# Optimization experiments

Measured on AMD Instinct MI355X. Metric: run time of the kernel, lower is better.

## Reference

```python
import jax, jax.numpy as jnp
import numpy as np

B, T, C = 16, 4096, 64  # batch, seq_len, n_embd == head_size


def setup_inputs() -> dict:
    key = jax.random.key(0)
    k1, k2, k3, k4 = jax.random.split(key, 4)
    x = jax.random.normal(k1, (B, T, C), dtype=jnp.float32)
    Wq = jax.random.normal(k2, (C, C), dtype=jnp.float32) * (C ** -0.5)
    Wk = jax.random.normal(k3, (C, C), dtype=jnp.float32) * (C ** -0.5)
    Wv = jax.random.normal(k4, (C, C), dtype=jnp.float32) * (C ** -0.5)
    return {"x": x, "Wq": Wq, "Wk": Wk, "Wv": Wv}


def reference(x, Wq, Wk, Wv):
    # Single-head causal self-attention (dropout rate = 0.0 in source -> identity).
    q = jnp.einsum('btc,cd->btd', x, Wq)  # [B,T,D]
    k = jnp.einsum('btc,cd->btd', x, Wk)  # [B,T,D]
    v = jnp.einsum('btc,cd->btd', x, Wv)  # [B,T,D]
    scale = q.shape[-1] ** -0.5
    wei = jnp.einsum('btd,bsd->bts', q, k) * scale  # [B,T,T] scores
    causal = jnp.tril(jnp.ones((T, T), dtype=bool))  # [T,T]
    wei = jnp.where(causal[None, :, :], wei, jnp.finfo(wei.dtype).min)
    wei = jax.nn.softmax(wei, axis=-1)
    out = jnp.einsum('bts,bsd->btd', wei, v)  # [B,T,D]
    return out
```

## Files before the change

### kernel.cpp

```cpp
#include <hip/hip_runtime.h>
#include <hip/hip_bf16.h>
#include <math.h>

#define BATCH 16
#define SEQ 4096
#define HDIM 64

typedef __attribute__((ext_vector_type(8))) short bf16x8;
typedef __attribute__((ext_vector_type(4))) float f32x4;
typedef __attribute__((ext_vector_type(4))) unsigned int u32x4;
typedef __attribute__((ext_vector_type(8))) unsigned short us8;

#define QSCALE 0.1803368801111601f

static __device__ __forceinline__ float exp2_fast(float x) {
#if __has_builtin(__builtin_amdgcn_exp2f)
    return __builtin_amdgcn_exp2f(x);
#else
    float r; asm("v_exp_f32 %0, %1" : "=v"(r) : "v"(x)); return r;
#endif
}

static __device__ __forceinline__ void load_lds16(const void* g, void* l) {
    __builtin_amdgcn_global_load_lds(
        (const __attribute__((address_space(1))) unsigned int*)g,
        (__attribute__((address_space(3))) unsigned int*)l,
        16, 0, 0);
}

static __device__ __forceinline__ unsigned short bf16bits(float f) {
    __hip_bfloat16 h = __float2bfloat16(f);
    return *(unsigned short*)&h;
}

static __device__ __forceinline__ unsigned int pack_bf16_trunc(float f0, float f1) {
    unsigned int u0 = __builtin_bit_cast(unsigned int, f0);
    unsigned int u1 = __builtin_bit_cast(unsigned int, f1);
#if __has_builtin(__builtin_amdgcn_perm)
    return __builtin_amdgcn_perm(u1, u0, 0x07060302u);
#else
    return (u1 & 0xFFFF0000u) | (u0 >> 16);
#endif
}

__global__ __launch_bounds__(256)
void qkv_mfma_kernel(const float* __restrict__ x,
                     const float* __restrict__ Wq,
                     const float* __restrict__ Wk,
                     const float* __restrict__ Wv,
                     __hip_bfloat16* __restrict__ qb,
                     __hip_bfloat16* __restrict__ kb,
                     __hip_bfloat16* __restrict__ vt) {
    __shared__ __attribute__((aligned(16))) __hip_bfloat16 swt[3 * 64 * 64];
    __shared__ __attribute__((aligned(16))) __hip_bfloat16 sout[64][80];
    const int tid = threadIdx.x;
    const int wv = tid >> 6;
    const int lane = tid & 63;
    const int quad = lane >> 4;
    const int ml = lane & 15;
    const size_t row0 = (size_t)blockIdx.x * 64;
    const int batch = (int)(row0 >> 12);
    const int t0 = (int)(row0 & 4095);

    #pragma unroll
    for (int mat = 0; mat < 3; ++mat) {
        const float* W = (mat == 0) ? Wq : (mat == 1) ? Wk : Wv;
        const float sc = (mat == 0) ? QSCALE : 1.0f;
        #pragma unroll
        for (int c2 = 0; c2 < 2; ++c2) {
            const int chunk = c2 * 256 + tid;
            const int n = chunk & 63;
            const int c = chunk >> 6;
            us8 u;
            #pragma unroll
            for (int j = 0; j < 8; ++j)
                u[j] = bf16bits(W[(c * 8 + j) * HDIM + n] * sc);
            *(us8*)(swt + mat * 4096 + n * 64 + (size_t)(c ^ (n & 7)) * 8) = u;
        }
    }

    bf16x8 a0, a1;
    {
        const float4* xr = (const float4*)(x + (row0 + wv * 16 + ml) * HDIM);
        float4 lo = xr[quad * 2], hi = xr[quad * 2 + 1];
        float t8[8] = {lo.x, lo.y, lo.z, lo.w, hi.x, hi.y, hi.z, hi.w};
        #pragma unroll
        for (int j = 0; j < 8; ++j) a0[j] = (short)bf16bits(t8[j]);
        lo = xr[8 + quad * 2]; hi = xr[9 + quad * 2];
        float u8[8] = {lo.x, lo.y, lo.z, lo.w, hi.x, hi.y, hi.z, hi.w};
        #pragma unroll
        for (int j = 0; j < 8; ++j) a1[j] = (short)bf16bits(u8[j]);
    }
    __syncthreads();

    #pragma unroll
    for (int mat = 0; mat < 3; ++mat) {
        const __hip_bfloat16* wb = swt + mat * 4096;
        f32x4 acc[4];
        #pragma unroll
        for (int nt = 0; nt < 4; ++nt) {
            const int n = nt * 16 + ml;
            const int nx = n & 7;
            const bf16x8 bl = *(const bf16x8*)(wb + (size_t)n * 64 + (size_t)((quad) ^ nx) * 8);
            const bf16x8 bh = *(const bf16x8*)(wb + (size_t)n * 64 + (size_t)((quad + 4) ^ nx) * 8);
            acc[nt] = __builtin_amdgcn_mfma_f32_16x16x32_bf16(a0, bl, (f32x4){0.f,0.f,0.f,0.f}, 0, 0, 0);
            acc[nt] = __builtin_amdgcn_mfma_f32_16x16x32_bf16(a1, bh, acc[nt], 0, 0, 0);
        }

        if (mat < 2) {
            #pragma unroll
            for (int nt = 0; nt < 4; ++nt)
                #pragma unroll
                for (int r = 0; r < 4; ++r)
                    sout[wv * 16 + quad * 4 + r][nt * 16 + ml] = __float2bfloat16(acc[nt][r]);
        } else {
            #pragma unroll
            for (int nt = 0; nt < 4; ++nt)
                #pragma unroll
                for (int r = 0; r < 4; ++r)
                    sout[nt * 16 + ml][(wv >> 1) * 32 + quad * 8 + (wv & 1) * 4 + r] =
                        __float2bfloat16(acc[nt][r]);
        }
        __syncthreads();
        __hip_bfloat16* dst = (mat == 0) ? qb : (mat == 1) ? kb : vt;
        #pragma unroll
        for (int c2 = 0; c2 < 2; ++c2) {
            const int cc = c2 * 256 + tid;
            const int row = cc >> 3, g = cc & 7;
            us8 u = *(const us8*)&sout[row][g * 8];
            if (mat < 2)
                *(us8*)(dst + (row0 + row) * HDIM + g * 8) = u;
            else
                *(us8*)(dst + ((size_t)batch * HDIM + row) * SEQ + t0 + g * 8) = u;
        }
        __syncthreads();
    }
}

__global__ __launch_bounds__(256, 4)
void flash_mfma_kernel(const __hip_bfloat16* __restrict__ qb,
                       const __hip_bfloat16* __restrict__ kbuf,
                       const __hip_bfloat16* __restrict__ vt,
                       float* __restrict__ out) {
    __shared__ __attribute__((aligned(16))) __hip_bfloat16 smem[16384];

    const int tid = threadIdx.x;
    const int wv = tid >> 6;
    const int lane = tid & 63;
    const int quad = lane >> 4;
    const int ml = lane & 15;
    const int mh = wv & 1;
    const int kh = wv >> 1;

    const int id = blockIdx.x;
    const int b = id & 15;
    const int t = id >> 4;
    const int hi2 = t >> 4, mid = t & 15;
    const int qt = (hi2 == 0) ? (63 - mid)
                 : (hi2 == 1) ? (32 + mid)
                 : (hi2 == 2) ? (31 - mid) : mid;
    const int qbw = qt * 64 + mh * 32;
    const size_t bb = (size_t)b * SEQ * HDIM;

    const __hip_bfloat16* Q = qb + bb;
    const __hip_bfloat16* K = kbuf + bb;
    const __hip_bfloat16* VT = vt + bb;

    bf16x8 bq[2][2];
    #pragma unroll
    for (int qi = 0; qi < 2; ++qi)
        #pragma unroll
        for (int h = 0; h < 2; ++h)
            bq[qi][h] = *(const bf16x8*)(Q + (size_t)(qbw + qi * 16 + ml) * HDIM + h * 32 + quad * 8);

    bf16x8 ones8;
    #pragma unroll
    for (int j = 0; j < 8; ++j) ones8[j] = (short)0x3F80;

    f32x4 acc[4][2];
    #pragma unroll
    for (int nt = 0; nt < 4; ++nt)
        #pragma unroll
        for (int qi = 0; qi < 2; ++qi) acc[nt][qi] = (f32x4){0.f, 0.f, 0.f, 0.f};
    f32x4 lacc[2] = {(f32x4){0.f,0.f,0.f,0.f}, (f32x4){0.f,0.f,0.f,0.f}};

    const int s0 = wv * 128 + lane;
    const int s1 = s0 + 64;
    const int r0row = s0 >> 3, r0ch = (s0 & 7) ^ (r0row & 7);
    const int r1row = s1 >> 3, r1ch = (s1 & 7) ^ (r1row & 7);
    const int d0 = (wv * 128) * 8;
    const int d1 = (wv * 128 + 64) * 8;

    int koff[2][2], voff[4];
    #pragma unroll
    for (int kt = 0; kt < 2; ++kt) {
        const int row = kh * 32 + kt * 16 + ml;
        const int rb = row << 3, rxx = row & 7;
        koff[kt][0] = (rb | (quad ^ rxx)) * 8;
        koff[kt][1] = (rb | ((quad + 4) ^ rxx)) * 8;
    }
    #pragma unroll
    for (int nt = 0; nt < 4; ++nt) {
        const int row = nt * 16 + ml;
        const int rb = row << 3, rxx = row & 7;
        voff[nt] = (rb | ((kh * 4 + quad) ^ rxx)) * 8;
    }

    load_lds16(K + (size_t)r0row * HDIM + r0ch * 8, smem + d0);
    load_lds16(K + (size_t)r1row * HDIM + r1ch * 8, smem + d1);
    load_lds16(VT + (size_t)r0row * SEQ + r0ch * 8, smem + 8192 + d0);
    load_lds16(VT + (size_t)r1row * SEQ + r1ch * 8, smem + 8192 + d1);
    asm volatile("s_waitcnt vmcnt(0)" ::: "memory");
    __syncthreads();

    for (int tile = 0; tile < qt; ++tile) {
        const int sel = (tile & 1) * 4096;
        const int nsel = 4096 - sel;
        const __hip_bfloat16* sk = smem + sel;
        const __hip_bfloat16* sv = smem + 8192 + sel;

        const int nk = tile * 64 + 64;
        load_lds16(K + (size_t)(nk + r0row) * HDIM + r0ch * 8, smem + nsel + d0);
        load_lds16(K + (size_t)(nk + r1row) * HDIM + r1ch * 8, smem + nsel + d1);
        load_lds16(VT + (size_t)r0row * SEQ + nk + r0ch * 8, smem + 8192 + nsel + d0);
        load_lds16(VT + (size_t)r1row * SEQ + nk + r1ch * 8, smem + 8192 + nsel + d1);

        bf16x8 kf[2][2], va[4];
        #pragma unroll
        for (int kt = 0; kt < 2; ++kt) {
            kf[kt][0] = *(const bf16x8*)(sk + koff[kt][0]);
            kf[kt][1] = *(const bf16x8*)(sk + koff[kt][1]);
        }
        #pragma unroll
        for (int nt = 0; nt < 4; ++nt)
            va[nt] = *(const bf16x8*)(sv + voff[nt]);

        f32x4 st[2][2];
        __builtin_amdgcn_s_setprio(1);
        #pragma unroll
        for (int kt = 0; kt < 2; ++kt)
            #pragma unroll
            for (int qi = 0; qi < 2; ++qi) {
                st[kt][qi] = __builtin_amdgcn_mfma_f32_16x16x32_bf16(kf[kt][0], bq[qi][0], (f32x4){0.f,0.f,0.f,0.f}, 0, 0, 0);
                st[kt][qi] = __builtin_amdgcn_mfma_f32_16x16x32_bf16(kf[kt][1], bq[qi][1], st[kt][qi], 0, 0, 0);
            }
        __builtin_amdgcn_s_setprio(0);

        bf16x8 p80;
        {
            float pv[8];
            #pragma unroll
            for (int half = 0; half < 2; ++half)
                #pragma unroll
                for (int r = 0; r < 4; ++r)
                    pv[half * 4 + r] = exp2_fast(st[half][0][r]);
            u32x4 pk;
            #pragma unroll
            for (int d = 0; d < 4; ++d)
                pk[d] = pack_bf16_trunc(pv[2 * d], pv[2 * d + 1]);
            p80 = __builtin_bit_cast(bf16x8, pk);
        }

        __builtin_amdgcn_s_setprio(1);
        lacc[0] = __builtin_amdgcn_mfma_f32_16x16x32_bf16(ones8, p80, lacc[0], 0, 0, 0);
        #pragma unroll
        for (int nt = 0; nt < 4; ++nt)
            acc[nt][0] = __builtin_amdgcn_mfma_f32_16x16x32_bf16(va[nt], p80, acc[nt][0], 0, 0, 0);
        __builtin_amdgcn_s_setprio(0);

        bf16x8 p81;
        {
            float pv[8];
            #pragma unroll
            for (int half = 0; half < 2; ++half)
                #pragma unroll
                for (int r = 0; r < 4; ++r)
                    pv[half * 4 + r] = exp2_fast(st[half][1][r]);
            u32x4 pk;
            #pragma unroll
            for (int d = 0; d < 4; ++d)
                pk[d] = pack_bf16_trunc(pv[2 * d], pv[2 * d + 1]);
            p81 = __builtin_bit_cast(bf16x8, pk);
        }

        __builtin_amdgcn_s_setprio(1);
        lacc[1] = __builtin_amdgcn_mfma_f32_16x16x32_bf16(ones8, p81, lacc[1], 0, 0, 0);
        #pragma unroll
        for (int nt = 0; nt < 4; ++nt)
            acc[nt][1] = __builtin_amdgcn_mfma_f32_16x16x32_bf16(va[nt], p81, acc[nt][1], 0, 0, 0);
        __builtin_amdgcn_s_setprio(0);

        asm volatile("s_waitcnt vmcnt(0)" ::: "memory");
        __syncthreads();
    }

    {
        const int kb0 = qt * 64;
        const int sel = (qt & 1) * 4096;
        const __hip_bfloat16* sk = smem + sel;
        const __hip_bfloat16* sv = smem + 8192 + sel;

        if (!(kh == 1 && mh == 0)) {
            bf16x8 kf[2][2], va[4];
            #pragma unroll
            for (int kt = 0; kt < 2; ++kt) {
                kf[kt][0] = *(const bf16x8*)(sk + koff[kt][0]);
                kf[kt][1] = *(const bf16x8*)(sk + koff[kt][1]);
            }
            #pragma unroll
            for (int nt = 0; nt < 4; ++nt)
                va[nt] = *(const bf16x8*)(sv + voff[nt]);

            f32x4 st[2][2];
            #pragma unroll
            for (int kt = 0; kt < 2; ++kt)
                #pragma unroll
                for (int qi = 0; qi < 2; ++qi) {
                    st[kt][qi] = __builtin_amdgcn_mfma_f32_16x16x32_bf16(kf[kt][0], bq[qi][0], (f32x4){0.f,0.f,0.f,0.f}, 0, 0, 0);
                    st[kt][qi] = __builtin_amdgcn_mfma_f32_16x16x32_bf16(kf[kt][1], bq[qi][1], st[kt][qi], 0, 0, 0);
                }

            bf16x8 p8[2];
            #pragma unroll
            for (int qi = 0; qi < 2; ++qi) {
                const int q = qbw + qi * 16 + ml;
                float pv[8];
                #pragma unroll
                for (int half = 0; half < 2; ++half)
                    #pragma unroll
                    for (int r = 0; r < 4; ++r) {
                        const int key = kb0 + kh * 32 + half * 16 + quad * 4 + r;
                        float pval = exp2_fast(st[half][qi][r]);
                        if (key > q) pval = 0.f;
                        pv[half * 4 + r] = pval;
                    }
                u32x4 pk;
                #pragma unroll
                for (int d = 0; d < 4; ++d)
                    pk[d] = pack_bf16_trunc(pv[2 * d], pv[2 * d + 1]);
                p8[qi] = __builtin_bit_cast(bf16x8, pk);
            }

            lacc[0] = __builtin_amdgcn_mfma_f32_16x16x32_bf16(ones8, p8[0], lacc[0], 0, 0, 0);
            lacc[1] = __builtin_amdgcn_mfma_f32_16x16x32_bf16(ones8, p8[1], lacc[1], 0, 0, 0);
            #pragma unroll
            for (int nt = 0; nt < 4; ++nt) {
                acc[nt][0] = __builtin_amdgcn_mfma_f32_16x16x32_bf16(va[nt], p8[0], acc[nt][0], 0, 0, 0);
                acc[nt][1] = __builtin_amdgcn_mfma_f32_16x16x32_bf16(va[nt], p8[1], acc[nt][1], 0, 0, 0);
            }
        }
    }

    float (*smerge)[64][18] = (float (*)[64][18])smem;
    #pragma unroll
    for (int qi = 0; qi < 2; ++qi) {
        __syncthreads();
        if (kh == 1) {
            float* mrow = smerge[mh][lane];
            #pragma unroll
            for (int nt = 0; nt < 4; ++nt)
                #pragma unroll
                for (int r = 0; r < 4; ++r) mrow[nt * 4 + r] = acc[nt][qi][r];
            mrow[16] = lacc[qi][0];
        }
        __syncthreads();
        if (kh == 0) {
            const float* mrow = smerge[mh][lane];
            const float inv = 1.0f / (lacc[qi][0] + mrow[16]);
            float* orow = out + bb + (size_t)(qbw + qi * 16 + ml) * HDIM;
            #pragma unroll
            for (int nt = 0; nt < 4; ++nt) {
                float4 o;
                o.x = (acc[nt][qi][0] + mrow[nt * 4 + 0]) * inv;
                o.y = (acc[nt][qi][1] + mrow[nt * 4 + 1]) * inv;
                o.z = (acc[nt][qi][2] + mrow[nt * 4 + 2]) * inv;
                o.w = (acc[nt][qi][3] + mrow[nt * 4 + 3]) * inv;
                *(float4*)(orow + nt * 16 + quad * 4) = o;
            }
        }
    }
}

extern "C" void kernel_launch(void* const* d_in, const int* in_sizes, int n_in,
                              void* d_out, int out_size, void* d_ws, size_t ws_size,
                              hipStream_t stream) {
    const float* x  = (const float*)d_in[0];
    const float* Wq = (const float*)d_in[1];
    const float* Wk = (const float*)d_in[2];
    const float* Wv = (const float*)d_in[3];
    float* outp = (float*)d_out;

    const size_t elems = (size_t)BATCH * SEQ * HDIM;
    __hip_bfloat16* qb = (__hip_bfloat16*)d_ws;
    __hip_bfloat16* kb = qb + elems;
    __hip_bfloat16* vt = kb + elems;

    qkv_mfma_kernel<<<dim3(BATCH * SEQ / 64), 256, 0, stream>>>(x, Wq, Wk, Wv, qb, kb, vt);
    flash_mfma_kernel<<<dim3(BATCH * SEQ / 64), 256, 0, stream>>>(qb, kb, vt, outp);
}
```

Baseline: 118.3 us.

## Precompute swizzled bf16 weights once and stage x via direct-to-LDS loads

Adds a tiny kernel that converts and swizzles Wq/Wk/Wv into bf16 in the workspace once per call, so the 1024 QKV blocks no longer each redo the strided fp32 weight reads and conversion. Each QKV block now pulls the pre-swizzled weights and its x tile into LDS with global_load_lds, then converts x to bf16 with truncating packs instead of round-to-nearest. This trades an extra kernel launch and one more workspace buffer for cheaper per-block setup, and truncation slightly changes the numerics of the x rounding.

After: 118.7 us. No clear change (+0.3%).

```diff
diff --git a/kernel.cpp b/kernel.cpp
--- a/kernel.cpp
+++ b/kernel.cpp
@@ -44,15 +44,38 @@
 }
 
 __global__ __launch_bounds__(256)
+void wconv_kernel(const float* __restrict__ Wq,
+                  const float* __restrict__ Wk,
+                  const float* __restrict__ Wv,
+                  __hip_bfloat16* __restrict__ wsw) {
+    const int mat = blockIdx.x;
+    const int tid = threadIdx.x;
+    const float* W = (mat == 0) ? Wq : (mat == 1) ? Wk : Wv;
+    const float sc = (mat == 0) ? QSCALE : 1.0f;
+    #pragma unroll
+    for (int c2 = 0; c2 < 2; ++c2) {
+        const int chunk = c2 * 256 + tid;
+        const int n = chunk & 63;
+        const int c = chunk >> 6;
+        us8 u;
+        #pragma unroll
+        for (int j = 0; j < 8; ++j)
+            u[j] = bf16bits(W[(c * 8 + j) * HDIM + n] * sc);
+        *(us8*)(wsw + mat * 4096 + n * 64 + (size_t)(c ^ (n & 7)) * 8) = u;
+    }
+}
+
+__global__ __launch_bounds__(256)
 void qkv_mfma_kernel(const float* __restrict__ x,
-                     const float* __restrict__ Wq,
-                     const float* __restrict__ Wk,
-                     const float* __restrict__ Wv,
+                     const __hip_bfloat16* __restrict__ wsw,
                      __hip_bfloat16* __restrict__ qb,
                      __hip_bfloat16* __restrict__ kb,
                      __hip_bfloat16* __restrict__ vt) {
     __shared__ __attribute__((aligned(16))) __hip_bfloat16 swt[3 * 64 * 64];
-    __shared__ __attribute__((aligned(16))) __hip_bfloat16 sout[64][80];
+    __shared__ __attribute__((aligned(16))) char spool[16384];
+    float* sx = (float*)spool;
+    __hip_bfloat16 (*sout)[80] = (__hip_bfloat16 (*)[80])spool;
+
     const int tid = threadIdx.x;
     const int wv = tid >> 6;
     const int lane = tid & 63;
@@ -63,33 +86,32 @@
     const int t0 = (int)(row0 & 4095);
 
     #pragma unroll
-    for (int mat = 0; mat < 3; ++mat) {
-        const float* W = (mat == 0) ? Wq : (mat == 1) ? Wk : Wv;
-        const float sc = (mat == 0) ? QSCALE : 1.0f;
-        #pragma unroll
-        for (int c2 = 0; c2 < 2; ++c2) {
-            const int chunk = c2 * 256 + tid;
-            const int n = chunk & 63;
-            const int c = chunk >> 6;
-            us8 u;
-            #pragma unroll
-            for (int j = 0; j < 8; ++j)
-                u[j] = bf16bits(W[(c * 8 + j) * HDIM + n] * sc);
-            *(us8*)(swt + mat * 4096 + n * 64 + (size_t)(c ^ (n & 7)) * 8) = u;
-        }
-    }
+    for (int r = 0; r < 6; ++r)
+        load_lds16(wsw + (size_t)(r * 256 + tid) * 8, swt + (size_t)(r * 256 + tid) * 8);
+    #pragma unroll
+    for (int r = 0; r < 4; ++r)
+        load_lds16(x + row0 * HDIM + (size_t)(r * 256 + tid) * 4, sx + (size_t)(r * 256 + tid) * 4);
+    asm volatile("s_waitcnt vmcnt(0)" ::: "memory");
+    __syncthreads();
 
     bf16x8 a0, a1;
     {
-        const float4* xr = (const float4*)(x + (row0 + wv * 16 + ml) * HDIM);
-        float4 lo = xr[quad * 2], hi = xr[quad * 2 + 1];
-        float t8[8] = {lo.x, lo.y, lo.z, lo.w, hi.x, hi.y, hi.z, hi.w};
-        #pragma unroll
-        for (int j = 0; j < 8; ++j) a0[j] = (short)bf16bits(t8[j]);
-        lo = xr[8 + quad * 2]; hi = xr[9 + quad * 2];
-        float u8[8] = {lo.x, lo.y, lo.z, lo.w, hi.x, hi.y, hi.z, hi.w};
-        #pragma unroll
-        for (int j = 0; j < 8; ++j) a1[j] = (short)bf16bits(u8[j]);
+        const float* xr = sx + (size_t)(wv * 16 + ml) * HDIM + quad * 8;
+        f32x4 lo = *(const f32x4*)xr;
+        f32x4 hi = *(const f32x4*)(xr + 4);
+        u32x4 pk;
+        pk[0] = pack_bf16_trunc(lo[0], lo[1]);
+        pk[1] = pack_bf16_trunc(lo[2], lo[3]);
+        pk[2] = pack_bf16_trunc(hi[0], hi[1]);
+        pk[3] = pack_bf16_trunc(hi[2], hi[3]);
+        a0 = __builtin_bit_cast(bf16x8, pk);
+        lo = *(const f32x4*)(xr + 32);
+        hi = *(const f32x4*)(xr + 36);
+        pk[0] = pack_bf16_trunc(lo[0], lo[1]);
+        pk[1] = pack_bf16_trunc(lo[2], lo[3]);
+        pk[2] = pack_bf16_trunc(hi[0], hi[1]);
+        pk[3] = pack_bf16_trunc(hi[2], hi[3]);
+        a1 = __builtin_bit_cast(bf16x8, pk);
     }
     __syncthreads();
 
@@ -394,7 +416,9 @@
     __hip_bfloat16* qb = (__hip_bfloat16*)d_ws;
     __hip_bfloat16* kb = qb + elems;
     __hip_bfloat16* vt = kb + elems;
-
-    qkv_mfma_kernel<<<dim3(BATCH * SEQ / 64), 256, 0, stream>>>(x, Wq, Wk, Wv, qb, kb, vt);
+    __hip_bfloat16* wsw = vt + elems;
+
+    wconv_kernel<<<dim3(3), 256, 0, stream>>>(Wq, Wk, Wv, wsw);
+    qkv_mfma_kernel<<<dim3(BATCH * SEQ / 64), 256, 0, stream>>>(x, wsw, qb, kb, vt);
     flash_mfma_kernel<<<dim3(BATCH * SEQ / 64), 256, 0, stream>>>(qb, kb, vt, outp);
 }
```
